# Optimization experiments

Measured on AMD Instinct MI355X. Metric: run time of the kernel, lower is better.

Reference implementation:

```python
import jax, jax.numpy as jnp
import numpy as np

B, S, T = 32, 64, 64
E, H, V = 512, 512, 32000
HD = 2 * H  # decoder hidden size (bidirectional encoder)
NEG = -1e9


def _lstm_cell(x, h, c, Wih, Whh, bih, bhh):
    # torch.nn.LSTMCell gate order: i, f, g, o
    g = x @ Wih.T + bih + h @ Whh.T + bhh
    i, f, gg, o = jnp.split(g, 4, axis=-1)
    c = jax.nn.sigmoid(f) * c + jax.nn.sigmoid(i) * jnp.tanh(gg)
    h = jax.nn.sigmoid(o) * jnp.tanh(c)
    return h, c


def _run_lstm(x, Wih, Whh, bih, bhh, hsz):
    # x: (B, S, E) -> hidden states (B, S, hsz). Faithful to lstm_traverse
    # (zero initial state, forward traversal).
    b = x.shape[0]
    h0 = jnp.zeros((b, hsz), x.dtype)

    def step(carry, xt):
        h, c = _lstm_cell(xt, carry[0], carry[1], Wih, Whh, bih, bhh)
        return (h, c), h

    _, Hs = jax.lax.scan(step, (h0, h0), jnp.swapaxes(x, 0, 1))
    return jnp.swapaxes(Hs, 0, 1)


def setup_inputs() -> dict:
    key = jax.random.key(0)
    ks = jax.random.split(key, 20)
    sc = 0.05
    inp = {
        'src_tokens': jax.random.randint(ks[0], (B, S), 0, V).astype(jnp.int32),
        'src_lens': jax.random.randint(ks[1], (B,), 1, S + 1).astype(jnp.int32),
        'trg_tokens': jax.random.randint(ks[2], (B, T), 0, V).astype(jnp.int32),
        'trg_lens': jax.random.randint(ks[3], (B,), 2, T + 1).astype(jnp.int32),
        'src_emb': jax.random.normal(ks[4], (V, E), jnp.float32) * sc,
        'trg_emb': jax.random.normal(ks[5], (V, E), jnp.float32) * sc,
        # encoder forward cell
        'We_ih': jax.random.normal(ks[6], (4 * H, E), jnp.float32) * sc,
        'We_hh': jax.random.normal(ks[7], (4 * H, H), jnp.float32) * sc,
        'be_ih': jnp.zeros((4 * H,), jnp.float32),
        'be_hh': jnp.zeros((4 * H,), jnp.float32),
        # encoder 'reverse' cell (note: source code traverses forward too)
        'Wr_ih': jax.random.normal(ks[8], (4 * H, E), jnp.float32) * sc,
        'Wr_hh': jax.random.normal(ks[9], (4 * H, H), jnp.float32) * sc,
        'br_ih': jnp.zeros((4 * H,), jnp.float32),
        'br_hh': jnp.zeros((4 * H,), jnp.float32),
        # decoder cell (hidden = 2H)
        'Wd_ih': jax.random.normal(ks[10], (4 * HD, E), jnp.float32) * sc,
        'Wd_hh': jax.random.normal(ks[11], (4 * HD, HD), jnp.float32) * sc,
        'bd_ih': jnp.zeros((4 * HD,), jnp.float32),
        'bd_hh': jnp.zeros((4 * HD,), jnp.float32),
        # output projection: (h, context) -> vocab, in = 4H
        'W_out': jax.random.normal(ks[12], (V, 2 * HD), jnp.float32) * sc,
        'b_out': jnp.zeros((V,), jnp.float32),
    }
    return inp


def _forward(src_tokens, src_lens, trg_tokens, trg_lens,
             src_emb, trg_emb,
             We_ih, We_hh, be_ih, be_hh,
             Wr_ih, Wr_hh, br_ih, br_hh,
             Wd_ih, Wd_hh, bd_ih, bd_hh,
             W_out, b_out):
    # ---- encode ----
    x = src_emb[src_tokens]                                  # (B,S,E)
    Hf = _run_lstm(x, We_ih, We_hh, be_ih, be_hh, H)
    Hr = _run_lstm(x, Wr_ih, Wr_hh, br_ih, br_hh, H)         # forward traversal, as in source
    src_states = jnp.concatenate([Hf, Hr], axis=-1)          # (B,S,2H)
    bidx = jnp.arange(src_states.shape[0])
    final = src_states[bidx, src_lens - 1]                   # (B,2H)

    # ---- decode (teacher forcing, masked-softmax dot attention) ----
    src_mask = jnp.arange(S)[None, :] < src_lens[:, None]    # (B,S)
    h0 = final
    c0 = jnp.zeros_like(final)

    def step(carry, inputs):
        h, c = carry
        tok, tgt = inputs
        v = trg_emb[tok]                                     # (B,E)
        h, c = _lstm_cell(v, h, c, Wd_ih, Wd_hh, bd_ih, bd_hh)
        scores = jnp.einsum('bh,bsh->bs', h, src_states)
        attn = jax.nn.softmax(jnp.where(src_mask, scores, NEG), axis=-1)
        ctx = jnp.einsum('bs,bsh->bh', attn, src_states)     # (B,2H)
        logits = jnp.concatenate([h, ctx], axis=-1) @ W_out.T + b_out
        ls = jax.nn.log_softmax(logits, axis=-1)
        nll = -jnp.take_along_axis(ls, tgt[:, None], axis=-1)[:, 0]
        return (h, c), nll

    in_toks = jnp.swapaxes(trg_tokens[:, :-1], 0, 1)          # (T-1,B)
    tgts = jnp.swapaxes(trg_tokens[:, 1:], 0, 1)              # (T-1,B)
    _, nll = jax.lax.scan(step, (h0, c0), (in_toks, tgts))
    nll = jnp.swapaxes(nll, 0, 1)                             # (B,T-1)

    mask = (jnp.arange(T)[None, :] < trg_lens[:, None]).astype(nll.dtype)
    return jnp.sum(-nll * mask[:, 1:])


def reference(src_tokens, src_lens, trg_tokens, trg_lens,
              src_emb, trg_emb,
              We_ih, We_hh, be_ih, be_hh,
              Wr_ih, Wr_hh, br_ih, br_hh,
              Wd_ih, Wd_hh, bd_ih, bd_hh,
              W_out, b_out):
    return _forward(src_tokens, src_lens, trg_tokens, trg_lens,
                    src_emb, trg_emb,
                    We_ih, We_hh, be_ih, be_hh,
                    Wr_ih, Wr_hh, br_ih, br_hh,
                    Wd_ih, Wd_hh, bd_ih, bd_hh,
                    W_out, b_out)
```

## Files before the change

### kernel.cpp

```cpp
#include <hip/hip_runtime.h>
#include <math.h>

#define NB 32
#define NS 64
#define NT 64
#define NHD 1024
#define NV 32000
#define NR 2016
#define NCT 250
#define RECB 64

typedef unsigned short u16;
typedef __bf16 bf16x8 __attribute__((ext_vector_type(8)));
typedef float f32x4 __attribute__((ext_vector_type(4)));
typedef unsigned u32x4 __attribute__((ext_vector_type(4)));
#define MFMA16 __builtin_amdgcn_mfma_f32_16x16x32_bf16

__device__ __forceinline__ float sigmf(float x) { return 1.f / (1.f + expf(-x)); }
__device__ __forceinline__ u16 f2bf(float f) {
  union { float f; unsigned u; } v; v.f = f;
  unsigned r = v.u + 0x7FFFu + ((v.u >> 16) & 1u);
  return (u16)(r >> 16);
}
__device__ __forceinline__ float bf2f(u16 h) {
  union { unsigned u; float f; } v; v.u = ((unsigned)h) << 16; return v.f;
}

__device__ __forceinline__ u32x4 ldg_coh(const void* p) {
  u32x4 v;
  asm volatile("global_load_dwordx4 %0, %1, off sc0 sc1" : "=v"(v) : "v"(p));
  return v;
}
__device__ __forceinline__ void stg_coh_u32(void* p, unsigned v) {
  asm volatile("global_store_dword %0, %1, off sc0 sc1" :: "v"(p), "v"(v) : "memory");
}
__device__ __forceinline__ unsigned ldg_coh_u32_wait(const void* p) {
  unsigned v;
  asm volatile("global_load_dword %0, %1, off sc0 sc1\n\ts_waitcnt vmcnt(0)"
               : "=v"(v) : "v"(p) : "memory");
  return v;
}
__device__ __forceinline__ void vmwait0() {
  asm volatile("s_waitcnt vmcnt(0)" ::: "memory");
}

__device__ __forceinline__ void cvt8(const float* __restrict__ in, u16* __restrict__ out, long i) {
  float4 a = *(const float4*)(in + i);
  float4 b = *(const float4*)(in + i + 4);
  union { u16 h[8]; uint4 v; } u;
  u.h[0]=f2bf(a.x); u.h[1]=f2bf(a.y); u.h[2]=f2bf(a.z); u.h[3]=f2bf(a.w);
  u.h[4]=f2bf(b.x); u.h[5]=f2bf(b.y); u.h[6]=f2bf(b.z); u.h[7]=f2bf(b.w);
  *(uint4*)(out + i) = u.v;
}

__global__ __launch_bounds__(256) void prep_kernel(
    const int* __restrict__ src_tokens, const int* __restrict__ trg_tokens,
    const int* __restrict__ trg_lens,
    const float* __restrict__ src_emb, const float* __restrict__ trg_emb,
    const float* __restrict__ We_ih, const float* __restrict__ Wr_ih,
    const float* __restrict__ Wd_ih, const float* __restrict__ We_hh,
    const float* __restrict__ Wr_hh, const float* __restrict__ Wd_hh,
    u16* __restrict__ xsrcb, u16* __restrict__ xtrgb,
    u16* __restrict__ Wihe, u16* __restrict__ Wihr, u16* __restrict__ Wihd,
    u16* __restrict__ Wbf_e, u16* __restrict__ Wfragd,
    unsigned* __restrict__ rowmap, unsigned* __restrict__ mcnt, unsigned* __restrict__ flags) {
  int b = blockIdx.x, tid = threadIdx.x;
  if (b < 512) {
    int idx = b * 256 + tid;
    int m = idx >> 6, c8 = (idx & 63) * 8;
    const float4* s = (const float4*)(src_emb + (size_t)src_tokens[m] * 512 + c8);
    float4 a = s[0], bb = s[1];
    union { u16 h[8]; uint4 v; } u;
    u.h[0]=f2bf(a.x); u.h[1]=f2bf(a.y); u.h[2]=f2bf(a.z); u.h[3]=f2bf(a.w);
    u.h[4]=f2bf(bb.x); u.h[5]=f2bf(bb.y); u.h[6]=f2bf(bb.z); u.h[7]=f2bf(bb.w);
    *(uint4*)(xsrcb + (size_t)m * 512 + c8) = u.v;
  } else if (b < 1016) {
    int idx = (b - 512) * 256 + tid;
    int m = idx >> 6, c8 = (idx & 63) * 8;
    int t = m >> 5, bb2 = m & 31;
    int token = trg_tokens[bb2 * NT + t];
    const float4* s = (const float4*)(trg_emb + (size_t)token * 512 + c8);
    float4 a = s[0], bb = s[1];
    union { u16 h[8]; uint4 v; } u;
    u.h[0]=f2bf(a.x); u.h[1]=f2bf(a.y); u.h[2]=f2bf(a.z); u.h[3]=f2bf(a.w);
    u.h[4]=f2bf(bb.x); u.h[5]=f2bf(bb.y); u.h[6]=f2bf(bb.z); u.h[7]=f2bf(bb.w);
    *(uint4*)(xtrgb + (size_t)m * 512 + c8) = u.v;
  } else if (b < 1528) {
    cvt8(We_ih, Wihe, ((long)(b - 1016) * 256 + tid) * 8);
  } else if (b < 2040) {
    cvt8(Wr_ih, Wihr, ((long)(b - 1528) * 256 + tid) * 8);
  } else if (b < 3064) {
    cvt8(Wd_ih, Wihd, ((long)(b - 2040) * 256 + tid) * 8);
  } else if (b < 3576) {
    cvt8(We_hh, Wbf_e, ((long)(b - 3064) * 256 + tid) * 8);
  } else if (b < 4088) {
    cvt8(Wr_hh, Wbf_e + (size_t)2048 * 512, ((long)(b - 3576) * 256 + tid) * 8);
  } else if (b < 6136) {
    int idx = (b - 4088) * 256 + tid;
    int lane = idx & 63;
    int kk = (idx >> 6) & 31;
    int g = (idx >> 11) & 3;
    int jt = idx >> 13;
    int row = g * 1024 + jt * 16 + (lane & 15);
    int col = kk * 32 + (lane >> 4) * 8;
    const float4* s = (const float4*)(Wd_hh + (size_t)row * NHD + col);
    float4 a = s[0], bb = s[1];
    union { u16 h[8]; uint4 v; } u;
    u.h[0]=f2bf(a.x); u.h[1]=f2bf(a.y); u.h[2]=f2bf(a.z); u.h[3]=f2bf(a.w);
    u.h[4]=f2bf(bb.x); u.h[5]=f2bf(bb.y); u.h[6]=f2bf(bb.z); u.h[7]=f2bf(bb.w);
    *(uint4*)(Wfragd + (size_t)idx * 8) = u.v;
  } else if (b == 6136) {
    __shared__ unsigned P[32];
    for (int i = tid; i < 2048; i += 256) rowmap[i] = 0u;
    if (tid == 0) {
      unsigned acc = 0;
      for (int bb2 = 0; bb2 < 32; bb2++) {
        P[bb2] = acc;
        int L = trg_lens[bb2]; if (L > NT) L = NT;
        acc += (unsigned)(L - 1);
      }
      mcnt[0] = acc;
    }
    __syncthreads();
    for (int bb2 = 0; bb2 < 32; bb2++) {
      int L = trg_lens[bb2]; if (L > NT) L = NT;
      int Lb = L - 1;
      if (tid < Lb) rowmap[P[bb2] + tid] = (unsigned)(tid * 32 + bb2);
    }
  } else {
    flags[tid] = 0u;
  }
}

__global__ __launch_bounds__(256) void mfma_gemm3(
    const u16* __restrict__ xsrcb, const u16* __restrict__ xtrgb,
    const u16* __restrict__ Wihe, const u16* __restrict__ Wihr, const u16* __restrict__ Wihd,
    const float* __restrict__ be_ih, const float* __restrict__ be_hh,
    const float* __restrict__ br_ih, const float* __restrict__ br_hh,
    const float* __restrict__ bd_ih, const float* __restrict__ bd_hh,
    float* __restrict__ Aef, float* __restrict__ Aer, float* __restrict__ Ad) {
  int by = blockIdx.y;
  const u16 *A, *Bm; const float *b0, *b1; float* C; int M, N, colTile;
  if (by < 16)      { A = xsrcb; Bm = Wihe; b0 = be_ih; b1 = be_hh; C = Aef; M = 2048; N = 2048; colTile = by; }
  else if (by < 32) { A = xsrcb; Bm = Wihr; b0 = br_ih; b1 = br_hh; C = Aer; M = 2048; N = 2048; colTile = by - 16; }
  else              { A = xtrgb; Bm = Wihd; b0 = bd_ih; b1 = bd_hh; C = Ad;  M = NR;   N = 4096; colTile = by - 32; }
  int tid = threadIdx.x, wave = tid >> 6, lane = tid & 63;
  int r = lane & 15, q = lane >> 4;
  int mh = wave >> 1, nh = wave & 1;
  int rowbase = blockIdx.x * 128 + mh * 64;
  int colbase = colTile * 128 + nh * 64;
  f32x4 acc[4][4] = {};
  for (int k0 = 0; k0 < 512; k0 += 32) {
    bf16x8 a[4], b[4];
#pragma unroll
    for (int mt = 0; mt < 4; mt++) {
      int rb = rowbase + mt * 16 + r;
      if (rb >= M) rb = 0;
      a[mt] = *(const bf16x8*)(A + (size_t)rb * 512 + k0 + q * 8);
    }
#pragma unroll
    for (int nt = 0; nt < 4; nt++)
      b[nt] = *(const bf16x8*)(Bm + (size_t)(colbase + nt * 16 + r) * 512 + k0 + q * 8);
#pragma unroll
    for (int mt = 0; mt < 4; mt++)
#pragma unroll
      for (int nt = 0; nt < 4; nt++)
        acc[mt][nt] = MFMA16(a[mt], b[nt], acc[mt][nt], 0, 0, 0);
  }
#pragma unroll
  for (int nt = 0; nt < 4; nt++) {
    int gn = colbase + nt * 16 + r;
    float bb = b0[gn] + b1[gn];
#pragma unroll
    for (int mt = 0; mt < 4; mt++)
#pragma unroll
      for (int j = 0; j < 4; j++) {
        int gm = rowbase + mt * 16 + q * 4 + j;
        if (gm < M) C[(size_t)gm * N + gn] = acc[mt][nt][j] + bb;
      }
  }
}

#define ENC_H_OFF 65536
#define ENC_G_OFF 98304
#define DEC_G_OFF 65536
__global__ __launch_bounds__(256, 1) void recurrence_kernel(
    const u16* __restrict__ Wbf_e,
    const u16* __restrict__ Wfragd,
    const float* __restrict__ Aef, const float* __restrict__ Aer, const float* __restrict__ Ad,
    const int* __restrict__ src_lens,
    u16* __restrict__ ssb, float* __restrict__ hs_dec, u16* __restrict__ Ybf,
    u16* __restrict__ hbf_e,
    u16* __restrict__ hbf_d,
    unsigned* flags) {
  __shared__ __align__(16) char smem[107008];
  const int tid = threadIdx.x, bid = blockIdx.x;
  const int wave = tid >> 6, lane = tid & 63;
  const int r = lane & 15, q = lane >> 4;
  const int g = wave;
  const int ob = tid >> 3;
  const int oj = (tid & 7) * 2;
  const int slen_ob = src_lens[ob];
  unsigned tgt = 0;

#define FLAGBAR(fbase, fcnt)                                                        \
  do {                                                                              \
    tgt++;                                                                          \
    vmwait0();                                                                      \
    __syncthreads();                                                                \
    if (wave == 0) {                                                                \
      if (lane == 0) stg_coh_u32(flags + bid, tgt);                                 \
      unsigned fv = tgt;                                                            \
      do {                                                                          \
        if (lane < (fcnt)) fv = ldg_coh_u32_wait(flags + (fbase) + lane);           \
      } while (__any(fv < tgt));                                                    \
    }                                                                               \
    __syncthreads();                                                                \
  } while (0)

  {
    const int lstm = bid >> 5, jt = bid & 31;
    float* gates = (float*)(smem + ENC_G_OFF);
    for (int c = tid; c < 64 * 64; c += 256) {
      int lr = c >> 6, c8 = (c & 63) * 8;
      int grow = lstm * 2048 + (lr >> 4) * 512 + jt * 16 + (lr & 15);
      uint4 v = *(const uint4*)(Wbf_e + (size_t)grow * 512 + c8);
      *(uint4*)(smem + ((lr * 1024 + c8 * 2) ^ ((lr & 7) << 4))) = v;
    }
    const float* Ae = lstm ? Aer : Aef;
    const int jcol = jt * 16 + oj;
    float creg0 = 0.f, creg1 = 0.f;
    for (int t = 0; t < NS; t++) {
      size_t abase = ((size_t)ob * NS + t) * 2048;
      float2 vi = *(const float2*)(Ae + abase + jcol);
      float2 vf = *(const float2*)(Ae + abase + 512 + jcol);
      float2 vg = *(const float2*)(Ae + abase + 1024 + jcol);
      float2 vo = *(const float2*)(Ae + abase + 1536 + jcol);
      if (t == 0) {
        u32x4 z = {0u, 0u, 0u, 0u};
#pragma unroll
        for (int k = 0; k < 8; k++) {
          int c = tid + k * 256;
          int hr = c >> 6, seg = c & 63;
          *(u32x4*)(smem + (ENC_H_OFF + ((hr * 1024 + seg * 16) ^ ((hr & 7) << 4)))) = z;
        }
      } else {
        const u16* hsrc = hbf_e + ((size_t)(t & 1) * 2 + lstm) * 16384;
        u32x4 hv[8];
#pragma unroll
        for (int k = 0; k < 8; k++) hv[k] = ldg_coh(hsrc + (tid + k * 256) * 8);
        vmwait0();
#pragma unroll
        for (int k = 0; k < 8; k++) {
          int c = tid + k * 256;
          int hr = c >> 6, seg = c & 63;
          *(u32x4*)(smem + (ENC_H_OFF + ((hr * 1024 + seg * 16) ^ ((hr & 7) << 4)))) = hv[k];
        }
      }
      __syncthreads();
      f32x4 acc0 = {0.f,0.f,0.f,0.f}, acc1 = {0.f,0.f,0.f,0.f};
      for (int ks = 0; ks < 512; ks += 32) {
        int col2 = (ks + q * 8) * 2;
        int a0r = r, a1r = 16 + r, br = g * 16 + r;
        bf16x8 a0 = *(const bf16x8*)(smem + (ENC_H_OFF + ((a0r * 1024 + col2) ^ ((a0r & 7) << 4))));
        bf16x8 a1 = *(const bf16x8*)(smem + (ENC_H_OFF + ((a1r * 1024 + col2) ^ ((a1r & 7) << 4))));
        bf16x8 bf = *(const bf16x8*)(smem + ((br * 1024 + col2) ^ ((br & 7) << 4)));
        acc0 = MFMA16(a0, bf, acc0, 0, 0, 0);
        acc1 = MFMA16(a1, bf, acc1, 0, 0, 0);
      }
#pragma unroll
      for (int j = 0; j < 4; j++) {
        gates[(g * 32 + q * 4 + j) * 17 + r] = acc0[j];
        gates[(g * 32 + 16 + q * 4 + j) * 17 + r] = acc1[j];
      }
      __syncthreads();
      {
        float I0 = vi.x + gates[(0 * 32 + ob) * 17 + oj];
        float I1 = vi.y + gates[(0 * 32 + ob) * 17 + oj + 1];
        float F0 = vf.x + gates[(1 * 32 + ob) * 17 + oj];
        float F1 = vf.y + gates[(1 * 32 + ob) * 17 + oj + 1];
        float G0 = vg.x + gates[(2 * 32 + ob) * 17 + oj];
        float G1 = vg.y + gates[(2 * 32 + ob) * 17 + oj + 1];
        float O0 = vo.x + gates[(3 * 32 + ob) * 17 + oj];
        float O1 = vo.y + gates[(3 * 32 + ob) * 17 + oj + 1];
        float c0 = sigmf(F0) * creg0 + sigmf(I0) * tanhf(G0);
        float c1 = sigmf(F1) * creg1 + sigmf(I1) * tanhf(G1);
        float h0 = sigmf(O0) * tanhf(c0);
        float h1 = sigmf(O1) * tanhf(c1);
        creg0 = c0; creg1 = c1;
        unsigned hv2 = ((unsigned)f2bf(h1) << 16) | f2bf(h0);
        stg_coh_u32(hbf_e + ((size_t)((t + 1) & 1) * 2 + lstm) * 16384 + ob * 512 + jcol, hv2);
        *(unsigned*)(ssb + ((size_t)ob * NS + t) * NHD + lstm * 512 + jcol) = hv2;
        if (t == slen_ob - 1)
          stg_coh_u32(hbf_d + ob * NHD + lstm * 512 + jcol, hv2);
      }
      FLAGBAR(lstm * 32, 32);
    }
  }

  FLAGBAR(0, RECB);

  {
    const int jt = bid;
    const int jcol = jt * 16 + oj;
    float* gates = (float*)(smem + DEC_G_OFF);
    const u16* wbase = Wfragd + (size_t)(jt * 4 + g) * 16384;
    float cd0 = 0.f, cd1 = 0.f;
    for (int t = 0; t < NT - 1; t++) {
      const float* ad = Ad + ((size_t)t * NB + ob) * 4096;
      float2 vi = *(const float2*)(ad + jcol);
      float2 vf = *(const float2*)(ad + 1024 + jcol);
      float2 vg = *(const float2*)(ad + 2048 + jcol);
      float2 vo = *(const float2*)(ad + 3072 + jcol);
      const u16* hsrc = hbf_d + (size_t)(t & 1) * (32 * NHD);
      {
        u32x4 hv[16];
#pragma unroll
        for (int k = 0; k < 16; k++) hv[k] = ldg_coh(hsrc + (tid + k * 256) * 8);
        vmwait0();
#pragma unroll
        for (int k = 0; k < 16; k++) {
          int c = tid + k * 256;
          int hr = c >> 7, seg = c & 127;
          *(u32x4*)(smem + ((hr * 2048 + seg * 16) ^ ((hr & 7) << 4))) = hv[k];
        }
      }
      __syncthreads();
      f32x4 acc0 = {0.f,0.f,0.f,0.f}, acc1 = {0.f,0.f,0.f,0.f};
      for (int kk = 0; kk < 32; kk++) {
        int colb = (kk * 32 + q * 8) * 2;
        int a0r = r, a1r = 16 + r;
        bf16x8 a0 = *(const bf16x8*)(smem + ((a0r * 2048 + colb) ^ ((a0r & 7) << 4)));
        bf16x8 a1 = *(const bf16x8*)(smem + ((a1r * 2048 + colb) ^ ((a1r & 7) << 4)));
        bf16x8 bf = *(const bf16x8*)(wbase + ((size_t)kk * 64 + lane) * 8);
        acc0 = MFMA16(a0, bf, acc0, 0, 0, 0);
        acc1 = MFMA16(a1, bf, acc1, 0, 0, 0);
      }
#pragma unroll
      for (int j = 0; j < 4; j++) {
        gates[(g * 32 + q * 4 + j) * 17 + r] = acc0[j];
        gates[(g * 32 + 16 + q * 4 + j) * 17 + r] = acc1[j];
      }
      __syncthreads();
      {
        float I0 = vi.x + gates[(0 * 32 + ob) * 17 + oj];
        float I1 = vi.y + gates[(0 * 32 + ob) * 17 + oj + 1];
        float F0 = vf.x + gates[(1 * 32 + ob) * 17 + oj];
        float F1 = vf.y + gates[(1 * 32 + ob) * 17 + oj + 1];
        float G0 = vg.x + gates[(2 * 32 + ob) * 17 + oj];
        float G1 = vg.y + gates[(2 * 32 + ob) * 17 + oj + 1];
        float O0 = vo.x + gates[(3 * 32 + ob) * 17 + oj];
        float O1 = vo.y + gates[(3 * 32 + ob) * 17 + oj + 1];
        float c0 = sigmf(F0) * cd0 + sigmf(I0) * tanhf(G0);
        float c1 = sigmf(F1) * cd1 + sigmf(I1) * tanhf(G1);
        float h0 = sigmf(O0) * tanhf(c0);
        float h1 = sigmf(O1) * tanhf(c1);
        cd0 = c0; cd1 = c1;
        size_t rowY = (size_t)t * NB + ob;
        unsigned hv2 = ((unsigned)f2bf(h1) << 16) | f2bf(h0);
        stg_coh_u32(hbf_d + (size_t)((t + 1) & 1) * (32 * NHD) + ob * NHD + jcol, hv2);
        *(unsigned*)(Ybf + rowY * 2048 + jcol) = hv2;
        float2 hvf; hvf.x = h0; hvf.y = h1;
        *(float2*)(hs_dec + rowY * NHD + jcol) = hvf;
      }
      if (t != NT - 2) FLAGBAR(0, RECB);
    }
  }
#undef FLAGBAR
}

__global__ __launch_bounds__(256) void attn_kernel(const float* __restrict__ hs,
                                                   const u16* __restrict__ ssb,
                                                   const int* __restrict__ src_lens,
                                                   const unsigned* __restrict__ rowmap,
                                                   const unsigned* __restrict__ mcnt,
                                                   const float* __restrict__ W_out,
                                                   u16* __restrict__ Wofrag,
                                                   u16* __restrict__ Ybf) {
  __shared__ __align__(16) float hsh[NHD];
  __shared__ float sc[NS];
  __shared__ float att[NS];
  int tid = threadIdx.x;
  if (blockIdx.x >= NR) {
    long c0 = (long)(blockIdx.x - NR) * 64000;
    for (long idx = c0 + tid; idx < c0 + 64000; idx += 256) {
      int lane2 = (int)(idx & 63);
      int kk = (int)((idx >> 6) & 63);
      long j16 = idx >> 12;
      long row = j16 * 16 + (lane2 & 15);
      int col = kk * 32 + (lane2 >> 4) * 8;
      const float4* s = (const float4*)(W_out + (size_t)row * 2048 + col);
      float4 a = s[0], b = s[1];
      union { u16 h[8]; uint4 v; } u;
      u.h[0]=f2bf(a.x); u.h[1]=f2bf(a.y); u.h[2]=f2bf(a.z); u.h[3]=f2bf(a.w);
      u.h[4]=f2bf(b.x); u.h[5]=f2bf(b.y); u.h[6]=f2bf(b.z); u.h[7]=f2bf(b.w);
      *(uint4*)(Wofrag + (size_t)idx * 8) = u.v;
    }
    return;
  }
  int cr = blockIdx.x;
  if ((unsigned)cr >= mcnt[0]) return;
  int rr = (int)rowmap[cr];
  int b = rr & 31;
  for (int i = tid; i < NHD; i += 256) hsh[i] = hs[(size_t)rr * NHD + i];
  __syncthreads();
  {
    int s = tid >> 2, q = tid & 3;
    const u16* row = ssb + ((size_t)b * NS + s) * NHD + q * 256;
    const float* h4 = hsh + q * 256;
    float p = 0.f;
    for (int k = 0; k < 256; k += 8) {
      uint4 v = *(const uint4*)(row + k);
      p += h4[k + 0] * bf2f((u16)(v.x & 0xFFFF)) + h4[k + 1] * bf2f((u16)(v.x >> 16));
      p += h4[k + 2] * bf2f((u16)(v.y & 0xFFFF)) + h4[k + 3] * bf2f((u16)(v.y >> 16));
      p += h4[k + 4] * bf2f((u16)(v.z & 0xFFFF)) + h4[k + 5] * bf2f((u16)(v.z >> 16));
      p += h4[k + 6] * bf2f((u16)(v.w & 0xFFFF)) + h4[k + 7] * bf2f((u16)(v.w >> 16));
    }
    p += __shfl_xor(p, 1);
    p += __shfl_xor(p, 2);
    if (q == 0) sc[s] = (s < src_lens[b]) ? p : -1e9f;
  }
  __syncthreads();
  if (tid < 64) {
    float v = sc[tid];
    float m = v;
#pragma unroll
    for (int off = 1; off < 64; off <<= 1) m = fmaxf(m, __shfl_xor(m, off));
    float e = expf(v - m);
    float ssum = e;
#pragma unroll
    for (int off = 1; off < 64; off <<= 1) ssum += __shfl_xor(ssum, off);
    att[tid] = e / ssum;
  }
  __syncthreads();
  float a0 = 0, a1 = 0, a2 = 0, a3 = 0;
  int d = tid * 4;
  for (int s2 = 0; s2 < NS; s2++) {
    float a = att[s2];
    uint2 v = *(const uint2*)(ssb + ((size_t)b * NS + s2) * NHD + d);
    a0 += a * bf2f((u16)(v.x & 0xFFFF));
    a1 += a * bf2f((u16)(v.x >> 16));
    a2 += a * bf2f((u16)(v.y & 0xFFFF));
    a3 += a * bf2f((u16)(v.y >> 16));
  }
  ushort4 o;
  o.x = f2bf(a0); o.y = f2bf(a1); o.z = f2bf(a2); o.w = f2bf(a3);
  *(ushort4*)(Ybf + (size_t)rr * 2048 + NHD + d) = o;
}

__global__ void yfrag_repack(const u16* __restrict__ Ybf, const unsigned* __restrict__ rowmap,
                             u16* __restrict__ out) {
  int idx = blockIdx.x * 256 + threadIdx.x;
  if (idx >= 128 * 64 * 64) return;
  int lane = idx & 63;
  int kk = (idx >> 6) & 63;
  int im = idx >> 12;
  int rr = (int)rowmap[im * 16 + (lane & 15)];
  int col = kk * 32 + (lane >> 4) * 8;
  *(uint4*)(out + (size_t)idx * 8) = *(const uint4*)(Ybf + (size_t)rr * 2048 + col);
}

__global__ __launch_bounds__(256) void gemmlse_mfma(
    const u16* __restrict__ Yf,
    const u16* __restrict__ Wf,
    const float* __restrict__ bo, const int* __restrict__ trg_tok,
    const unsigned* __restrict__ rowmap, const unsigned* __restrict__ mcnt,
    float* __restrict__ pm, float* __restrict__ ps, float* __restrict__ tgtlog) {
  __shared__ int tgtc[128];
  __shared__ float pmp[2][128];
  __shared__ float psp[2][128];
  int o = blockIdx.x;
  int u = (o & 7) * 500 + (o >> 3);
  int bm = u & 15, bn = u >> 4;
  const int M = (int)mcnt[0];
  if (bm * 128 >= M) return;
  int tid = threadIdx.x;
  int wave = tid >> 6, lane = tid & 63;
  int r = lane & 15, q = lane >> 4;
  int mh = wave >> 1, nh = wave & 1;
  if (tid < 128) {
    int gm = bm * 128 + tid;
    if (gm < M) {
      int rr = (int)rowmap[gm];
      int tt = rr >> 5, b = rr & 31;
      tgtc[tid] = trg_tok[b * NT + tt + 1];
    } else {
      tgtc[tid] = -1;
    }
  }
  __syncthreads();
  const u16* ybase = Yf + (((size_t)(bm * 8 + mh * 4) * 64) * 64 + lane) * 8;
  const u16* wbase = Wf + (((size_t)(bn * 8 + nh * 4) * 64) * 64 + lane) * 8;
  f32x4 acc[4][4] = {};
  for (int kk = 0; kk < 64; kk += 2) {
    bf16x8 aA[4], bA[4], aB[4], bB[4];
#pragma unroll
    for (int mt = 0; mt < 4; mt++) {
      const u16* p = ybase + ((size_t)mt * 64 + kk) * 512;
      aA[mt] = *(const bf16x8*)(p);
      aB[mt] = *(const bf16x8*)(p + 512);
    }
#pragma unroll
    for (int nt = 0; nt < 4; nt++) {
      const u16* p = wbase + ((size_t)nt * 64 + kk) * 512;
      bA[nt] = *(const bf16x8*)(p);
      bB[nt] = *(const bf16x8*)(p + 512);
    }
#pragma unroll
    for (int mt = 0; mt < 4; mt++)
#pragma unroll
      for (int nt = 0; nt < 4; nt++)
        acc[mt][nt] = MFMA16(aA[mt], bA[nt], acc[mt][nt], 0, 0, 0);
#pragma unroll
    for (int mt = 0; mt < 4; mt++)
#pragma unroll
      for (int nt = 0; nt < 4; nt++)
        acc[mt][nt] = MFMA16(aB[mt], bB[nt], acc[mt][nt], 0, 0, 0);
  }
  int colbase = bn * 128 + nh * 64;
  float bo4[4];
#pragma unroll
  for (int nt = 0; nt < 4; nt++) bo4[nt] = bo[colbase + nt * 16 + r];
#pragma unroll
  for (int mt = 0; mt < 4; mt++)
#pragma unroll
    for (int nt = 0; nt < 4; nt++)
#pragma unroll
      for (int j = 0; j < 4; j++) acc[mt][nt][j] += bo4[nt];
#pragma unroll
  for (int mt = 0; mt < 4; mt++) {
#pragma unroll
    for (int j = 0; j < 4; j++) {
      float m = fmaxf(fmaxf(acc[mt][0][j], acc[mt][1][j]), fmaxf(acc[mt][2][j], acc[mt][3][j]));
      m = fmaxf(m, __shfl_xor(m, 1));
      m = fmaxf(m, __shfl_xor(m, 2));
      m = fmaxf(m, __shfl_xor(m, 4));
      m = fmaxf(m, __shfl_xor(m, 8));
      float s = expf(acc[mt][0][j] - m) + expf(acc[mt][1][j] - m) +
                expf(acc[mt][2][j] - m) + expf(acc[mt][3][j] - m);
      s += __shfl_xor(s, 1);
      s += __shfl_xor(s, 2);
      s += __shfl_xor(s, 4);
      s += __shfl_xor(s, 8);
      int lrow = mh * 64 + mt * 16 + q * 4 + j;
      if (r == 0) { pmp[nh][lrow] = m; psp[nh][lrow] = s; }
      int tc = tgtc[lrow];
      int off = tc - (bn * 128 + nh * 64);
      if (off >= 0 && off < 64 && (off & 15) == r) {
        tgtlog[bm * 128 + lrow] = acc[mt][off >> 4][j];
      }
    }
  }
  __syncthreads();
  if (tid < 128) {
    int gm = bm * 128 + tid;
    if (gm < M) {
      float m0 = pmp[0][tid], m1 = pmp[1][tid];
      float m = fmaxf(m0, m1);
      float s = psp[0][tid] * expf(m0 - m) + psp[1][tid] * expf(m1 - m);
      pm[(size_t)bn * NR + gm] = m;
      ps[(size_t)bn * NR + gm] = s;
    }
  }
}

__global__ void lse_combine_kernel(const float* __restrict__ pm, const float* __restrict__ ps,
                                   const float* __restrict__ tgtlog,
                                   const unsigned* __restrict__ mcnt,
                                   float* __restrict__ rowval) {
  int cr = blockIdx.x * blockDim.x + threadIdx.x;
  if (cr >= NR) return;
  if ((unsigned)cr >= mcnt[0]) { rowval[cr] = 0.f; return; }
  float m = -1e30f;
  for (int i = 0; i < NCT; i++) m = fmaxf(m, pm[(size_t)i * NR + cr]);
  float s = 0.f;
  for (int i = 0; i < NCT; i++) s += ps[(size_t)i * NR + cr] * expf(pm[(size_t)i * NR + cr] - m);
  float lse = m + logf(s);
  rowval[cr] = tgtlog[cr] - lse;
}

__global__ void final_reduce_kernel(const float* __restrict__ rowval, float* __restrict__ out) {
  __shared__ float sm[256];
  float s = 0.f;
  for (int i = threadIdx.x; i < NR; i += 256) s += rowval[i];
  sm[threadIdx.x] = s;
  __syncthreads();
  for (int off = 128; off > 0; off >>= 1) {
    if (threadIdx.x < off) sm[threadIdx.x] += sm[threadIdx.x + off];
    __syncthreads();
  }
  if (threadIdx.x == 0) out[0] = sm[0];
}

extern "C" void kernel_launch(void* const* d_in, const int* in_sizes, int n_in,
                              void* d_out, int out_size, void* d_ws, size_t ws_size,
                              hipStream_t stream) {
  const int* src_tokens = (const int*)d_in[0];
  const int* src_lens = (const int*)d_in[1];
  const int* trg_tokens = (const int*)d_in[2];
  const int* trg_lens = (const int*)d_in[3];
  const float* src_emb = (const float*)d_in[4];
  const float* trg_emb = (const float*)d_in[5];
  const float* We_ih = (const float*)d_in[6];
  const float* We_hh = (const float*)d_in[7];
  const float* be_ih = (const float*)d_in[8];
  const float* be_hh = (const float*)d_in[9];
  const float* Wr_ih = (const float*)d_in[10];
  const float* Wr_hh = (const float*)d_in[11];
  const float* br_ih = (const float*)d_in[12];
  const float* br_hh = (const float*)d_in[13];
  const float* Wd_ih = (const float*)d_in[14];
  const float* Wd_hh = (const float*)d_in[15];
  const float* bd_ih = (const float*)d_in[16];
  const float* bd_hh = (const float*)d_in[17];
  const float* W_out = (const float*)d_in[18];
  const float* b_out = (const float*)d_in[19];

  char* base = (char*)d_ws;
  size_t off = 0;
  auto alloc = [&](size_t bytes) -> char* {
    char* p = base + off;
    off += (bytes + 255) & ~(size_t)255;
    return p;
  };
  u16* xsrcb = (u16*)alloc((size_t)2048 * 512 * 2);
  u16* xtrgb = (u16*)alloc((size_t)NR * 512 * 2);
  u16* Wihe = (u16*)alloc((size_t)2048 * 512 * 2);
  u16* Wihr = (u16*)alloc((size_t)2048 * 512 * 2);
  u16* Wihd = (u16*)alloc((size_t)4096 * 512 * 2);
  u16* Wbf_e = (u16*)alloc((size_t)4096 * 512 * 2);
  u16* Wfragd = (u16*)alloc((size_t)4096 * 1024 * 2);
  u16* Wofrag = (u16*)alloc((size_t)NV * 2048 * 2);
  u16* Yfrag = (u16*)alloc((size_t)128 * 64 * 64 * 8 * 2);
  float* Aef = (float*)alloc((size_t)2048 * 2048 * 4);
  float* Aer = (float*)alloc((size_t)2048 * 2048 * 4);
  float* Ad  = (float*)alloc((size_t)NR * 4096 * 4);
  u16* ssb  = (u16*)alloc((size_t)NB * NS * NHD * 2);
  float* hs_dec = (float*)alloc((size_t)NR * NHD * 4);
  u16* Ybf = (u16*)alloc((size_t)NR * 2048 * 2);
  u16* hbf_e = (u16*)alloc((size_t)4 * 32 * 512 * 2);
  u16* hbf_d = (u16*)alloc((size_t)2 * 32 * NHD * 2);
  float* pm = (float*)alloc((size_t)NCT * NR * 4);
  float* ps = (float*)alloc((size_t)NCT * NR * 4);
  float* tgtlog = (float*)alloc((size_t)NR * 4);
  float* rowval = (float*)alloc((size_t)NR * 4);
  unsigned* flags = (unsigned*)alloc(1024);
  unsigned* rowmap = (unsigned*)alloc(2048 * 4);
  unsigned* mcnt = (unsigned*)alloc(256);

  prep_kernel<<<6138, 256, 0, stream>>>(
      src_tokens, trg_tokens, trg_lens, src_emb, trg_emb,
      We_ih, Wr_ih, Wd_ih, We_hh, Wr_hh, Wd_hh,
      xsrcb, xtrgb, Wihe, Wihr, Wihd, Wbf_e, Wfragd, rowmap, mcnt, flags);

  mfma_gemm3<<<dim3(16, 64), 256, 0, stream>>>(
      xsrcb, xtrgb, Wihe, Wihr, Wihd,
      be_ih, be_hh, br_ih, br_hh, bd_ih, bd_hh, Aef, Aer, Ad);

  recurrence_kernel<<<RECB, 256, 0, stream>>>(Wbf_e, Wfragd, Aef, Aer, Ad, src_lens,
                                              ssb, hs_dec, Ybf, hbf_e, hbf_d, flags);

  attn_kernel<<<NR + 128, 256, 0, stream>>>(hs_dec, ssb, src_lens, rowmap, mcnt,
                                            W_out, Wofrag, Ybf);

  yfrag_repack<<<2048, 256, 0, stream>>>(Ybf, rowmap, Yfrag);

  gemmlse_mfma<<<4000, 256, 0, stream>>>(Yfrag, Wofrag, b_out, trg_tokens, rowmap, mcnt, pm, ps, tgtlog);
  lse_combine_kernel<<<(NR + 255) / 256, 256, 0, stream>>>(pm, ps, tgtlog, mcnt, rowval);
  final_reduce_kernel<<<1, 256, 0, stream>>>(rowval, (float*)d_out);
}
```

Baseline: 1.408 ms.

## Drop fp32 decoder hidden copy and move W_out conversion to standalone kernel

The recurrence kernel no longer writes an fp32 copy of each decoder hidden state. The attention kernel now reads the bf16 hidden state already stored in Ybf, which removes one global write stream from the serial recurrence and halves the attention input read. The W_out fp32-to-bf16 fragment conversion moves out of the tail blocks of the attention kernel into its own fully parallel kernel launched before the GEMMs. The cost is lower precision for the attention query (bf16 instead of fp32) and one extra kernel launch. Ybf is passed as both input and output of attn_kernel, which is safe only if the kernel reads and writes different column ranges.

After: 1.263 ms. 10.3% less time.

```diff
diff --git a/kernel.cpp b/kernel.cpp
--- a/kernel.cpp
+++ b/kernel.cpp
@@ -132,6 +132,22 @@
   }
 }
 
+__global__ void cvt_wo_frag(const float* __restrict__ W, u16* __restrict__ out) {
+  long idx = (long)blockIdx.x * 256 + threadIdx.x;
+  if (idx >= (long)2000 * 64 * 64) return;
+  int lane = (int)(idx & 63);
+  int kk = (int)((idx >> 6) & 63);
+  long j16 = idx >> 12;
+  long row = j16 * 16 + (lane & 15);
+  int col = kk * 32 + (lane >> 4) * 8;
+  const float4* s = (const float4*)(W + (size_t)row * 2048 + col);
+  float4 a = s[0], b = s[1];
+  union { u16 h[8]; uint4 v; } u;
+  u.h[0]=f2bf(a.x); u.h[1]=f2bf(a.y); u.h[2]=f2bf(a.z); u.h[3]=f2bf(a.w);
+  u.h[4]=f2bf(b.x); u.h[5]=f2bf(b.y); u.h[6]=f2bf(b.z); u.h[7]=f2bf(b.w);
+  *(uint4*)(out + (size_t)idx * 8) = u.v;
+}
+
 __global__ __launch_bounds__(256) void mfma_gemm3(
     const u16* __restrict__ xsrcb, const u16* __restrict__ xtrgb,
     const u16* __restrict__ Wihe, const u16* __restrict__ Wihr, const u16* __restrict__ Wihd,
@@ -189,7 +205,7 @@
     const u16* __restrict__ Wfragd,
     const float* __restrict__ Aef, const float* __restrict__ Aer, const float* __restrict__ Ad,
     const int* __restrict__ src_lens,
-    u16* __restrict__ ssb, float* __restrict__ hs_dec, u16* __restrict__ Ybf,
+    u16* __restrict__ ssb, u16* __restrict__ Ybf,
     u16* __restrict__ hbf_e,
     u16* __restrict__ hbf_d,
     unsigned* flags) {
@@ -360,8 +376,6 @@
         unsigned hv2 = ((unsigned)f2bf(h1) << 16) | f2bf(h0);
         stg_coh_u32(hbf_d + (size_t)((t + 1) & 1) * (32 * NHD) + ob * NHD + jcol, hv2);
         *(unsigned*)(Ybf + rowY * 2048 + jcol) = hv2;
-        float2 hvf; hvf.x = h0; hvf.y = h1;
-        *(float2*)(hs_dec + rowY * NHD + jcol) = hvf;
       }
       if (t != NT - 2) FLAGBAR(0, RECB);
     }
@@ -369,40 +383,28 @@
 #undef FLAGBAR
 }
 
-__global__ __launch_bounds__(256) void attn_kernel(const float* __restrict__ hs,
+__global__ __launch_bounds__(256) void attn_kernel(const u16* __restrict__ Ybf_in,
                                                    const u16* __restrict__ ssb,
                                                    const int* __restrict__ src_lens,
                                                    const unsigned* __restrict__ rowmap,
                                                    const unsigned* __restrict__ mcnt,
-                                                   const float* __restrict__ W_out,
-                                                   u16* __restrict__ Wofrag,
                                                    u16* __restrict__ Ybf) {
   __shared__ __align__(16) float hsh[NHD];
   __shared__ float sc[NS];
   __shared__ float att[NS];
-  int tid = threadIdx.x;
-  if (blockIdx.x >= NR) {
-    long c0 = (long)(blockIdx.x - NR) * 64000;
-    for (long idx = c0 + tid; idx < c0 + 64000; idx += 256) {
-      int lane2 = (int)(idx & 63);
-      int kk = (int)((idx >> 6) & 63);
-      long j16 = idx >> 12;
-      long row = j16 * 16 + (lane2 & 15);
-      int col = kk * 32 + (lane2 >> 4) * 8;
-      const float4* s = (const float4*)(W_out + (size_t)row * 2048 + col);
-      float4 a = s[0], b = s[1];
-      union { u16 h[8]; uint4 v; } u;
-      u.h[0]=f2bf(a.x); u.h[1]=f2bf(a.y); u.h[2]=f2bf(a.z); u.h[3]=f2bf(a.w);
-      u.h[4]=f2bf(b.x); u.h[5]=f2bf(b.y); u.h[6]=f2bf(b.z); u.h[7]=f2bf(b.w);
-      *(uint4*)(Wofrag + (size_t)idx * 8) = u.v;
-    }
-    return;
-  }
   int cr = blockIdx.x;
   if ((unsigned)cr >= mcnt[0]) return;
   int rr = (int)rowmap[cr];
   int b = rr & 31;
-  for (int i = tid; i < NHD; i += 256) hsh[i] = hs[(size_t)rr * NHD + i];
+  int tid = threadIdx.x;
+  {
+    int i = tid * 4;
+    uint2 v = *(const uint2*)(Ybf_in + (size_t)rr * 2048 + i);
+    hsh[i + 0] = bf2f((u16)(v.x & 0xFFFF));
+    hsh[i + 1] = bf2f((u16)(v.x >> 16));
+    hsh[i + 2] = bf2f((u16)(v.y & 0xFFFF));
+    hsh[i + 3] = bf2f((u16)(v.y >> 16));
+  }
   __syncthreads();
   {
     int s = tid >> 2, q = tid & 3;
@@ -636,7 +638,6 @@
   float* Aer = (float*)alloc((size_t)2048 * 2048 * 4);
   float* Ad  = (float*)alloc((size_t)NR * 4096 * 4);
   u16* ssb  = (u16*)alloc((size_t)NB * NS * NHD * 2);
-  float* hs_dec = (float*)alloc((size_t)NR * NHD * 4);
   u16* Ybf = (u16*)alloc((size_t)NR * 2048 * 2);
   u16* hbf_e = (u16*)alloc((size_t)4 * 32 * 512 * 2);
   u16* hbf_d = (u16*)alloc((size_t)2 * 32 * NHD * 2);
@@ -653,15 +654,16 @@
       We_ih, Wr_ih, Wd_ih, We_hh, Wr_hh, Wd_hh,
       xsrcb, xtrgb, Wihe, Wihr, Wihd, Wbf_e, Wfragd, rowmap, mcnt, flags);
 
+  cvt_wo_frag<<<32000, 256, 0, stream>>>(W_out, Wofrag);
+
   mfma_gemm3<<<dim3(16, 64), 256, 0, stream>>>(
       xsrcb, xtrgb, Wihe, Wihr, Wihd,
       be_ih, be_hh, br_ih, br_hh, bd_ih, bd_hh, Aef, Aer, Ad);
 
   recurrence_kernel<<<RECB, 256, 0, stream>>>(Wbf_e, Wfragd, Aef, Aer, Ad, src_lens,
-                                              ssb, hs_dec, Ybf, hbf_e, hbf_d, flags);
-
-  attn_kernel<<<NR + 128, 256, 0, stream>>>(hs_dec, ssb, src_lens, rowmap, mcnt,
-                                            W_out, Wofrag, Ybf);
+                                              ssb, Ybf, hbf_e, hbf_d, flags);
+
+  attn_kernel<<<NR, 256, 0, stream>>>(Ybf, ssb, src_lens, rowmap, mcnt, Ybf);
 
   yfrag_repack<<<2048, 256, 0, stream>>>(Ybf, rowmap, Yfrag);
 
```
